# Performance work log

Measured on AMD Instinct MI355X. Metric: run time of the kernel, lower is better.

## Reference

```python
import jax, jax.numpy as jnp
import numpy as np
from jax import lax

B, HIST, FC, N, F = 64, 24, 24, 1000, 8
EMB, HID, NEMB, OUT = 32, 64, 1000, 1
IN = EMB + OUT  # GRU input dim


def setup_inputs() -> dict:
    key = jax.random.key(0)
    ks = jax.random.split(key, 11)
    X = jax.random.normal(ks[0], (B, HIST + FC, N, F), jnp.float32)
    idx = jax.random.randint(ks[1], (B, HIST + FC, N), 0, NEMB)
    X = X.at[..., -1].set(idx.astype(jnp.float32))  # last channel = spatial ids
    hn = jax.random.normal(ks[2], (B * N, HID), jnp.float32)
    xn = jax.random.normal(ks[3], (B, N, OUT), jnp.float32)
    s = 0.1
    emb_table = jax.random.normal(ks[4], (NEMB, EMB), jnp.float32) * s
    W_ih = jax.random.normal(ks[5], (3 * HID, IN), jnp.float32) * s
    W_hh = jax.random.normal(ks[6], (3 * HID, HID), jnp.float32) * s
    b_ih = jax.random.normal(ks[7], (3 * HID,), jnp.float32) * s
    b_hh = jax.random.normal(ks[8], (3 * HID,), jnp.float32) * s
    W_out = jax.random.normal(ks[9], (OUT, HID), jnp.float32) * s
    b_out = jax.random.normal(ks[10], (OUT,), jnp.float32) * s
    return {"X": X, "hn": hn, "xn": xn, "emb_table": emb_table,
            "W_ih": W_ih, "W_hh": W_hh, "b_ih": b_ih, "b_hh": b_hh,
            "W_out": W_out, "b_out": b_out}


def reference(X, hn, xn, emb_table, W_ih, W_hh, b_ih, b_hh, W_out, b_out):
    # indices for the forecast steps: [FC, B, N]
    idx_seq = X[:, :FC, :, -1].astype(jnp.int32).transpose(1, 0, 2)

    def step(carry, idx_t):
        h, x_prev = carry                      # h: [B*N, HID], x_prev: [B, N, 1]
        emb = emb_table[idx_t]                 # [B, N, EMB] gather
        x = jnp.concatenate([x_prev, emb], axis=-1).reshape(B * N, IN)
        gi = x @ W_ih.T + b_ih                 # [B*N, 3*HID]
        gh = h @ W_hh.T + b_hh
        i_r, i_z, i_n = jnp.split(gi, 3, axis=-1)
        h_r, h_z, h_n = jnp.split(gh, 3, axis=-1)
        r = jax.nn.sigmoid(i_r + h_r)
        z = jax.nn.sigmoid(i_z + h_z)
        n = jnp.tanh(i_n + r * h_n)
        h_new = (1.0 - z) * n + z * h
        out = h_new.reshape(B, N, HID) @ W_out.T + b_out  # [B, N, 1]
        return (h_new, out), out

    _, preds = lax.scan(step, (hn, xn), idx_seq)  # preds: [FC, B, N, 1]
    return preds.transpose(1, 0, 2, 3)            # [B, FC, N, 1]
```

## Files before the change

kernel.cpp:

```cpp
#include <hip/hip_runtime.h>
#include <math.h>

#define BB   64
#define FC   24
#define NN   1000
#define HID  64
#define EMBD 32
#define TT   48
#define FF   8
#define NEMB 1000
#define G3   192
#define INSZ 33

#define CPB  32
#define TPB  256
#define MT   2
#define AST  72
#define XST  32

typedef __attribute__((ext_vector_type(8))) short bf16x8;
typedef __attribute__((ext_vector_type(4))) float f32x4;

static __device__ __forceinline__ unsigned short f2bf(float f) {
    unsigned u = __builtin_bit_cast(unsigned, f);
    u += 0x7FFFu + ((u >> 16) & 1u);
    return (unsigned short)(u >> 16);
}
static __device__ __forceinline__ unsigned cvt_pk_bf16(float a, float b) {
    unsigned r;
    asm("v_cvt_pk_bf16_f32 %0, %1, %2" : "=v"(r) : "v"(a), "v"(b));
    return r;
}
static __device__ __forceinline__ float fast_sigmoid(float v) {
    float e = __builtin_amdgcn_exp2f(-1.4426950408889634f * v);
    return __builtin_amdgcn_rcpf(1.0f + e);
}
static __device__ __forceinline__ float fast_tanh(float v) {
    float vv = fminf(fmaxf(v, -15.0f), 15.0f);
    float e = __builtin_amdgcn_exp2f(2.8853900817779268f * vv);
    return 1.0f - 2.0f * __builtin_amdgcn_rcpf(e + 1.0f);
}

static __device__ __forceinline__ void lds_barrier() {
    __builtin_amdgcn_sched_barrier(0);
    asm volatile("s_waitcnt lgkmcnt(0)" ::: "memory");
    __builtin_amdgcn_s_barrier();
    __builtin_amdgcn_sched_barrier(0);
}

__global__ __launch_bounds__(TPB) __attribute__((amdgpu_waves_per_eu(3)))
void gru_decoder(
    const float* __restrict__ X,
    const float* __restrict__ hn0,
    const float* __restrict__ xn,
    const float* __restrict__ emb,
    const float* __restrict__ Wih,
    const float* __restrict__ Whh,
    const float* __restrict__ bih,
    const float* __restrict__ bhh,
    const float* __restrict__ Wout,
    const float* __restrict__ bout,
    float* __restrict__ out)
{
    __shared__ __align__(16) unsigned short Abuf[CPB * AST];
    __shared__ __align__(16) unsigned short Xt[2][CPB * XST];
    __shared__ int   idxbuf[FC * CPB];
    __shared__ float xbuf[CPB];

    const int tid  = threadIdx.x;
    const int lane = tid & 63;
    const int g    = tid >> 6;
    const int quad = lane >> 4;
    const int l15  = lane & 15;
    const int jcol = g * 16 + l15;
    const int rowb = quad * 4;
    const int cell0 = blockIdx.x * CPB;

    for (int e = tid; e < FC * CPB; e += TPB) {
        int t = e >> 5, m = e & 31;
        int cell = cell0 + m;
        int b = cell / NN, n = cell - b * NN;
        idxbuf[t * CPB + m] = (int)X[(((size_t)b * TT + t) * NN + n) * FF + 7];
    }
    if (tid < CPB) xbuf[tid] = xn[cell0 + tid];

    bf16x8 Bf[3][2];
    #pragma unroll
    for (int gate = 0; gate < 3; ++gate) {
        #pragma unroll
        for (int ks = 0; ks < 2; ++ks) {
            const float* src = Whh + (size_t)(gate * HID + jcol) * HID + ks * 32 + quad * 8;
            float4 lo = *(const float4*)src;
            float4 hi = *(const float4*)(src + 4);
            bf16x8 f;
            f[0] = (short)f2bf(lo.x); f[1] = (short)f2bf(lo.y);
            f[2] = (short)f2bf(lo.z); f[3] = (short)f2bf(lo.w);
            f[4] = (short)f2bf(hi.x); f[5] = (short)f2bf(hi.y);
            f[6] = (short)f2bf(hi.z); f[7] = (short)f2bf(hi.w);
            Bf[gate][ks] = f;
        }
    }
    bf16x8 BX[3];
    #pragma unroll
    for (int gate = 0; gate < 3; ++gate) {
        const float* src = Wih + (size_t)(gate * HID + jcol) * INSZ + 1 + quad * 8;
        bf16x8 f;
        #pragma unroll
        for (int e = 0; e < 8; ++e) f[e] = (short)f2bf(src[e]);
        BX[gate] = f;
    }

    const float w0r = Wih[(size_t)jcol * INSZ];
    const float w0z = Wih[(size_t)(HID + jcol) * INSZ];
    const float w0n = Wih[(size_t)(2 * HID + jcol) * INSZ];
    const float br  = bih[jcol] + bhh[jcol];
    const float bz  = bih[HID + jcol] + bhh[HID + jcol];
    const float bni = bih[2 * HID + jcol];
    const float bhn = bhh[2 * HID + jcol];
    const f32x4 cr  = {br,  br,  br,  br };
    const f32x4 cz  = {bz,  bz,  bz,  bz };
    const f32x4 cni = {bni, bni, bni, bni};
    const f32x4 cng = {bhn, bhn, bhn, bhn};
    const float bout0 = bout[0];

    const int cd_m   = g * 8 + (lane & 7);
    const int kslice = lane >> 3;
    float wout_r[8];
    #pragma unroll
    for (int e2 = 0; e2 < 8; ++e2) wout_r[e2] = Wout[kslice * 8 + e2];
    const int cd_cell = cell0 + cd_m;
    const int cd_b = cd_cell / NN, cd_n = cd_cell - cd_b * NN;
    const size_t obase = (size_t)cd_b * FC * NN + cd_n;

    float hold[MT][4];
    #pragma unroll
    for (int mt = 0; mt < MT; ++mt) {
        #pragma unroll
        for (int rr = 0; rr < 4; ++rr) {
            int m = mt * 16 + rowb + rr;
            float h = hn0[((size_t)cell0 + m) * HID + jcol];
            hold[mt][rr] = h;
            Abuf[m * AST + jcol] = f2bf(h);
        }
    }
    __syncthreads();

    const int r8 = tid >> 3, k4 = (tid & 7) * 4;
    {
        int idx = idxbuf[r8];
        float4 e4 = *(const float4*)(emb + (size_t)idx * EMBD + k4);
        unsigned p0 = cvt_pk_bf16(e4.x, e4.y);
        unsigned p1 = cvt_pk_bf16(e4.z, e4.w);
        *(uint2*)&Xt[0][r8 * XST + k4] = make_uint2(p0, p1);
    }
    __syncthreads();

    for (int t = 0; t < FC; ++t) {
        const int tn = (t + 1 < FC) ? t + 1 : FC - 1;
        const int nidx = idxbuf[tn * CPB + r8];
        const float4 e4 = *(const float4*)(emb + (size_t)nidx * EMBD + k4);

        const unsigned short* Xc = Xt[t & 1];

        f32x4 accr[MT], accz[MT], accni[MT], accng[MT];
        #pragma unroll
        for (int mt = 0; mt < MT; ++mt) {
            const bf16x8 a0 = *(const bf16x8*)&Abuf[(mt * 16 + l15) * AST + quad * 8];
            const bf16x8 a1 = *(const bf16x8*)&Abuf[(mt * 16 + l15) * AST + 32 + quad * 8];
            const bf16x8 x0 = *(const bf16x8*)&Xc[(mt * 16 + l15) * XST + quad * 8];
            accr[mt]  = __builtin_amdgcn_mfma_f32_16x16x32_bf16(x0, BX[0], cr, 0, 0, 0);
            accr[mt]  = __builtin_amdgcn_mfma_f32_16x16x32_bf16(a0, Bf[0][0], accr[mt], 0, 0, 0);
            accr[mt]  = __builtin_amdgcn_mfma_f32_16x16x32_bf16(a1, Bf[0][1], accr[mt], 0, 0, 0);
            accz[mt]  = __builtin_amdgcn_mfma_f32_16x16x32_bf16(x0, BX[1], cz, 0, 0, 0);
            accz[mt]  = __builtin_amdgcn_mfma_f32_16x16x32_bf16(a0, Bf[1][0], accz[mt], 0, 0, 0);
            accz[mt]  = __builtin_amdgcn_mfma_f32_16x16x32_bf16(a1, Bf[1][1], accz[mt], 0, 0, 0);
            accni[mt] = __builtin_amdgcn_mfma_f32_16x16x32_bf16(x0, BX[2], cni, 0, 0, 0);
            accng[mt] = __builtin_amdgcn_mfma_f32_16x16x32_bf16(a0, Bf[2][0], cng, 0, 0, 0);
            accng[mt] = __builtin_amdgcn_mfma_f32_16x16x32_bf16(a1, Bf[2][1], accng[mt], 0, 0, 0);
        }

        if (t > 0) {
            bf16x8 hv = *(const bf16x8*)&Abuf[cd_m * AST + kslice * 8];
            const unsigned* hv32 = (const unsigned*)&hv;
            float o = 0.f;
            #pragma unroll
            for (int q = 0; q < 4; ++q) {
                unsigned v = hv32[q];
                o = fmaf(wout_r[2 * q],     __builtin_bit_cast(float, v << 16),         o);
                o = fmaf(wout_r[2 * q + 1], __builtin_bit_cast(float, v & 0xFFFF0000u), o);
            }
            o += __shfl_xor(o, 8);
            o += __shfl_xor(o, 16);
            o += __shfl_xor(o, 32);
            if (lane < 8) {
                float oo = o + bout0;
                out[obase + (size_t)(t - 1) * NN] = oo;
                xbuf[cd_m] = oo;
            }
        }
        lds_barrier();

        #pragma unroll
        for (int mt = 0; mt < MT; ++mt) {
            #pragma unroll
            for (int rp = 0; rp < 2; ++rp) {
                float h2[2];
                #pragma unroll
                for (int k = 0; k < 2; ++k) {
                    const int rr = rp * 2 + k;
                    const int m  = mt * 16 + rowb + rr;
                    float xp = xbuf[m];
                    float r  = fast_sigmoid(fmaf(w0r, xp, accr[mt][rr]));
                    float z  = fast_sigmoid(fmaf(w0z, xp, accz[mt][rr]));
                    float nv = fast_tanh(fmaf(r, accng[mt][rr],
                                              fmaf(w0n, xp, accni[mt][rr])));
                    float hnew = nv + z * (hold[mt][rr] - nv);
                    hold[mt][rr] = hnew;
                    h2[k] = hnew;
                }
                unsigned pk = cvt_pk_bf16(h2[0], h2[1]);
                const int m0 = mt * 16 + rowb + rp * 2;
                Abuf[m0 * AST + jcol]       = (unsigned short)pk;
                Abuf[(m0 + 1) * AST + jcol] = (unsigned short)(pk >> 16);
            }
        }

        {
            unsigned p0 = cvt_pk_bf16(e4.x, e4.y);
            unsigned p1 = cvt_pk_bf16(e4.z, e4.w);
            *(uint2*)&Xt[(t + 1) & 1][r8 * XST + k4] = make_uint2(p0, p1);
        }
        lds_barrier();
    }

    {
        bf16x8 hv = *(const bf16x8*)&Abuf[cd_m * AST + kslice * 8];
        const unsigned* hv32 = (const unsigned*)&hv;
        float o = 0.f;
        #pragma unroll
        for (int q = 0; q < 4; ++q) {
            unsigned v = hv32[q];
            o = fmaf(wout_r[2 * q],     __builtin_bit_cast(float, v << 16),         o);
            o = fmaf(wout_r[2 * q + 1], __builtin_bit_cast(float, v & 0xFFFF0000u), o);
        }
        o += __shfl_xor(o, 8);
        o += __shfl_xor(o, 16);
        o += __shfl_xor(o, 32);
        if (lane < 8) out[obase + (size_t)(FC - 1) * NN] = o + bout0;
    }
}

extern "C" void kernel_launch(void* const* d_in, const int* in_sizes, int n_in,
                              void* d_out, int out_size, void* d_ws, size_t ws_size,
                              hipStream_t stream) {
    (void)in_sizes; (void)n_in; (void)out_size; (void)d_ws; (void)ws_size;
    const float* X    = (const float*)d_in[0];
    const float* hn   = (const float*)d_in[1];
    const float* xn   = (const float*)d_in[2];
    const float* emb  = (const float*)d_in[3];
    const float* Wih  = (const float*)d_in[4];
    const float* Whh  = (const float*)d_in[5];
    const float* bih  = (const float*)d_in[6];
    const float* bhh  = (const float*)d_in[7];
    const float* Wout = (const float*)d_in[8];
    const float* bout = (const float*)d_in[9];
    float* out = (float*)d_out;

    const int blocks = (BB * NN) / CPB;
    gru_decoder<<<blocks, TPB, 0, stream>>>(X, hn, xn, emb, Wih, Whh,
                                            bih, bhh, Wout, bout, out);
}
```

Baseline: 265.1 us.

## Software-pipeline GRU row halves across barriers and fold log2e into weights

```diff
diff --git a/kernel.cpp b/kernel.cpp
--- a/kernel.cpp
+++ b/kernel.cpp
@@ -8,15 +8,15 @@
 #define EMBD 32
 #define TT   48
 #define FF   8
-#define NEMB 1000
-#define G3   192
 #define INSZ 33
 
 #define CPB  32
 #define TPB  256
-#define MT   2
 #define AST  72
-#define XST  32
+#define XST  40
+
+#define NL2E (-1.4426950408889634f)
+#define TL2E ( 2.8853900817779268f)
 
 typedef __attribute__((ext_vector_type(8))) short bf16x8;
 typedef __attribute__((ext_vector_type(4))) float f32x4;
@@ -31,14 +31,13 @@
     asm("v_cvt_pk_bf16_f32 %0, %1, %2" : "=v"(r) : "v"(a), "v"(b));
     return r;
 }
-static __device__ __forceinline__ float fast_sigmoid(float v) {
-    float e = __builtin_amdgcn_exp2f(-1.4426950408889634f * v);
-    return __builtin_amdgcn_rcpf(1.0f + e);
-}
-static __device__ __forceinline__ float fast_tanh(float v) {
-    float vv = fminf(fmaxf(v, -15.0f), 15.0f);
-    float e = __builtin_amdgcn_exp2f(2.8853900817779268f * vv);
-    return 1.0f - 2.0f * __builtin_amdgcn_rcpf(e + 1.0f);
+static __device__ __forceinline__ bf16x8 mk_bf8(float4 lo, float4 hi, float s) {
+    union { unsigned u[4]; bf16x8 v; } r;
+    r.u[0] = cvt_pk_bf16(lo.x * s, lo.y * s);
+    r.u[1] = cvt_pk_bf16(lo.z * s, lo.w * s);
+    r.u[2] = cvt_pk_bf16(hi.x * s, hi.y * s);
+    r.u[3] = cvt_pk_bf16(hi.z * s, hi.w * s);
+    return r.v;
 }
 
 static __device__ __forceinline__ void lds_barrier() {
@@ -87,61 +86,55 @@
     bf16x8 Bf[3][2];
     #pragma unroll
     for (int gate = 0; gate < 3; ++gate) {
+        const float s = (gate < 2) ? NL2E : TL2E;
         #pragma unroll
         for (int ks = 0; ks < 2; ++ks) {
             const float* src = Whh + (size_t)(gate * HID + jcol) * HID + ks * 32 + quad * 8;
-            float4 lo = *(const float4*)src;
-            float4 hi = *(const float4*)(src + 4);
-            bf16x8 f;
-            f[0] = (short)f2bf(lo.x); f[1] = (short)f2bf(lo.y);
-            f[2] = (short)f2bf(lo.z); f[3] = (short)f2bf(lo.w);
-            f[4] = (short)f2bf(hi.x); f[5] = (short)f2bf(hi.y);
-            f[6] = (short)f2bf(hi.z); f[7] = (short)f2bf(hi.w);
-            Bf[gate][ks] = f;
+            Bf[gate][ks] = mk_bf8(*(const float4*)src, *(const float4*)(src + 4), s);
         }
     }
     bf16x8 BX[3];
     #pragma unroll
     for (int gate = 0; gate < 3; ++gate) {
+        const float s = (gate < 2) ? NL2E : TL2E;
         const float* src = Wih + (size_t)(gate * HID + jcol) * INSZ + 1 + quad * 8;
-        bf16x8 f;
+        union { unsigned u[4]; bf16x8 v; } f;
         #pragma unroll
-        for (int e = 0; e < 8; ++e) f[e] = (short)f2bf(src[e]);
-        BX[gate] = f;
-    }
-
-    const float w0r = Wih[(size_t)jcol * INSZ];
-    const float w0z = Wih[(size_t)(HID + jcol) * INSZ];
-    const float w0n = Wih[(size_t)(2 * HID + jcol) * INSZ];
-    const float br  = bih[jcol] + bhh[jcol];
-    const float bz  = bih[HID + jcol] + bhh[HID + jcol];
-    const float bni = bih[2 * HID + jcol];
-    const float bhn = bhh[2 * HID + jcol];
-    const f32x4 cr  = {br,  br,  br,  br };
-    const f32x4 cz  = {bz,  bz,  bz,  bz };
-    const f32x4 cni = {bni, bni, bni, bni};
-    const f32x4 cng = {bhn, bhn, bhn, bhn};
+        for (int p = 0; p < 4; ++p)
+            f.u[p] = cvt_pk_bf16(src[2 * p] * s, src[2 * p + 1] * s);
+        BX[gate] = f.v;
+    }
+
+    const float w0r2 = NL2E * Wih[(size_t)jcol * INSZ];
+    const float w0z2 = NL2E * Wih[(size_t)(HID + jcol) * INSZ];
+    const float w0n2 = TL2E * Wih[(size_t)(2 * HID + jcol) * INSZ];
+    const float br2  = NL2E * (bih[jcol] + bhh[jcol]);
+    const float bz2  = NL2E * (bih[HID + jcol] + bhh[HID + jcol]);
+    const float bni2 = TL2E * bih[2 * HID + jcol];
+    const float bhn2 = TL2E * bhh[2 * HID + jcol];
     const float bout0 = bout[0];
 
-    const int cd_m   = g * 8 + (lane & 7);
-    const int kslice = lane >> 3;
-    float wout_r[8];
-    #pragma unroll
-    for (int e2 = 0; e2 < 8; ++e2) wout_r[e2] = Wout[kslice * 8 + e2];
-    const int cd_cell = cell0 + cd_m;
-    const int cd_b = cd_cell / NN, cd_n = cd_cell - cd_b * NN;
-    const size_t obase = (size_t)cd_b * FC * NN + cd_n;
-
-    float hold[MT][4];
-    #pragma unroll
-    for (int mt = 0; mt < MT; ++mt) {
-        #pragma unroll
-        for (int rr = 0; rr < 4; ++rr) {
-            int m = mt * 16 + rowb + rr;
-            float h = hn0[((size_t)cell0 + m) * HID + jcol];
-            hold[mt][rr] = h;
-            Abuf[m * AST + jcol] = f2bf(h);
-        }
+    float wout4[4];
+    #pragma unroll
+    for (int e2 = 0; e2 < 4; ++e2) wout4[e2] = Wout[l15 * 4 + e2];
+    const int od_c = g * 4 + quad;
+    size_t ob[2];
+    #pragma unroll
+    for (int gx = 0; gx < 2; ++gx) {
+        int cell = cell0 + gx * 16 + od_c;
+        int b = cell / NN, n = cell - b * NN;
+        ob[gx] = (size_t)b * FC * NN + n;
+    }
+
+    float hold0[4], hold1[4];
+    #pragma unroll
+    for (int rr = 0; rr < 4; ++rr) {
+        int m0 = rowb + rr, m1 = 16 + rowb + rr;
+        float h0 = hn0[((size_t)cell0 + m0) * HID + jcol];
+        float h1 = hn0[((size_t)cell0 + m1) * HID + jcol];
+        hold0[rr] = h0; hold1[rr] = h1;
+        Abuf[m0 * AST + jcol] = f2bf(h0);
+        Abuf[m1 * AST + jcol] = f2bf(h1);
     }
     __syncthreads();
 
@@ -149,105 +142,104 @@
     {
         int idx = idxbuf[r8];
         float4 e4 = *(const float4*)(emb + (size_t)idx * EMBD + k4);
-        unsigned p0 = cvt_pk_bf16(e4.x, e4.y);
-        unsigned p1 = cvt_pk_bf16(e4.z, e4.w);
-        *(uint2*)&Xt[0][r8 * XST + k4] = make_uint2(p0, p1);
+        *(uint2*)&Xt[0][r8 * XST + k4] =
+            make_uint2(cvt_pk_bf16(e4.x, e4.y), cvt_pk_bf16(e4.z, e4.w));
     }
     __syncthreads();
 
+    auto PHASE_A = [&](int X16, const unsigned short* Xc,
+                       f32x4& ar, f32x4& az, f32x4& ani, f32x4& ang) {
+        const bf16x8 a0 = *(const bf16x8*)&Abuf[(X16 + l15) * AST + quad * 8];
+        const bf16x8 a1 = *(const bf16x8*)&Abuf[(X16 + l15) * AST + 32 + quad * 8];
+        const bf16x8 x0 = *(const bf16x8*)&Xc[(X16 + l15) * XST + quad * 8];
+        const f32x4 z4 = {0.f, 0.f, 0.f, 0.f};
+        ar  = __builtin_amdgcn_mfma_f32_16x16x32_bf16(x0, BX[0], z4, 0, 0, 0);
+        ar  = __builtin_amdgcn_mfma_f32_16x16x32_bf16(a0, Bf[0][0], ar, 0, 0, 0);
+        ar  = __builtin_amdgcn_mfma_f32_16x16x32_bf16(a1, Bf[0][1], ar, 0, 0, 0);
+        az  = __builtin_amdgcn_mfma_f32_16x16x32_bf16(x0, BX[1], z4, 0, 0, 0);
+        az  = __builtin_amdgcn_mfma_f32_16x16x32_bf16(a0, Bf[1][0], az, 0, 0, 0);
+        az  = __builtin_amdgcn_mfma_f32_16x16x32_bf16(a1, Bf[1][1], az, 0, 0, 0);
+        ani = __builtin_amdgcn_mfma_f32_16x16x32_bf16(x0, BX[2], z4, 0, 0, 0);
+        ang = __builtin_amdgcn_mfma_f32_16x16x32_bf16(a0, Bf[2][0], z4, 0, 0, 0);
+        ang = __builtin_amdgcn_mfma_f32_16x16x32_bf16(a1, Bf[2][1], ang, 0, 0, 0);
+    };
+
+    auto PHASE_B = [&](int X16, f32x4& ar, f32x4& az, f32x4& ani, f32x4& ang,
+                       float* hold) {
+        #pragma unroll
+        for (int rp = 0; rp < 2; ++rp) {
+            float h2[2];
+            #pragma unroll
+            for (int k = 0; k < 2; ++k) {
+                const int rr = rp * 2 + k;
+                const int m  = X16 + rowb + rr;
+                const float xp = xbuf[m];
+                float sr = fmaf(w0r2, xp, ar[rr] + br2);
+                float r  = __builtin_amdgcn_rcpf(1.0f + __builtin_amdgcn_exp2f(sr));
+                float sz = fmaf(w0z2, xp, az[rr] + bz2);
+                float z  = __builtin_amdgcn_rcpf(1.0f + __builtin_amdgcn_exp2f(sz));
+                float v  = fmaf(r, ang[rr] + bhn2, fmaf(w0n2, xp, ani[rr] + bni2));
+                float e  = __builtin_amdgcn_exp2f(v);
+                float nv = fmaf(-2.0f, __builtin_amdgcn_rcpf(e + 1.0f), 1.0f);
+                float hnew = fmaf(z, hold[rr] - nv, nv);
+                hold[rr] = hnew;
+                h2[k] = hnew;
+            }
+            unsigned pk = cvt_pk_bf16(h2[0], h2[1]);
+            const int m0 = X16 + rowb + rp * 2;
+            Abuf[m0 * AST + jcol]       = (unsigned short)pk;
+            Abuf[(m0 + 1) * AST + jcol] = (unsigned short)(pk >> 16);
+        }
+    };
+
+    auto OUTDOT = [&](int gx, int tw, bool wr) {
+        const int X16 = gx << 4;
+        const uint2 hv = *(const uint2*)&Abuf[(X16 + od_c) * AST + l15 * 4];
+        float o;
+        o = wout4[0] * __builtin_bit_cast(float, hv.x << 16);
+        o = fmaf(wout4[1], __builtin_bit_cast(float, hv.x & 0xFFFF0000u), o);
+        o = fmaf(wout4[2], __builtin_bit_cast(float, hv.y << 16), o);
+        o = fmaf(wout4[3], __builtin_bit_cast(float, hv.y & 0xFFFF0000u), o);
+        o += __shfl_xor(o, 1);
+        o += __shfl_xor(o, 2);
+        o += __shfl_xor(o, 4);
+        o += __shfl_xor(o, 8);
+        if (l15 == 0) {
+            float oo = o + bout0;
+            out[ob[gx] + (size_t)tw * NN] = oo;
+            if (wr) xbuf[X16 + od_c] = oo;
+        }
+    };
+
+    f32x4 ar0, az0, ani0, ang0;
+    f32x4 ar1, az1, ani1, ang1;
+
+    #pragma unroll 2
     for (int t = 0; t < FC; ++t) {
         const int tn = (t + 1 < FC) ? t + 1 : FC - 1;
         const int nidx = idxbuf[tn * CPB + r8];
         const float4 e4 = *(const float4*)(emb + (size_t)nidx * EMBD + k4);
-
         const unsigned short* Xc = Xt[t & 1];
 
-        f32x4 accr[MT], accz[MT], accni[MT], accng[MT];
-        #pragma unroll
-        for (int mt = 0; mt < MT; ++mt) {
-            const bf16x8 a0 = *(const bf16x8*)&Abuf[(mt * 16 + l15) * AST + quad * 8];
-            const bf16x8 a1 = *(const bf16x8*)&Abuf[(mt * 16 + l15) * AST + 32 + quad * 8];
-            const bf16x8 x0 = *(const bf16x8*)&Xc[(mt * 16 + l15) * XST + quad * 8];
-            accr[mt]  = __builtin_amdgcn_mfma_f32_16x16x32_bf16(x0, BX[0], cr, 0, 0, 0);
-            accr[mt]  = __builtin_amdgcn_mfma_f32_16x16x32_bf16(a0, Bf[0][0], accr[mt], 0, 0, 0);
-            accr[mt]  = __builtin_amdgcn_mfma_f32_16x16x32_bf16(a1, Bf[0][1], accr[mt], 0, 0, 0);
-            accz[mt]  = __builtin_amdgcn_mfma_f32_16x16x32_bf16(x0, BX[1], cz, 0, 0, 0);
-            accz[mt]  = __builtin_amdgcn_mfma_f32_16x16x32_bf16(a0, Bf[1][0], accz[mt], 0, 0, 0);
-            accz[mt]  = __builtin_amdgcn_mfma_f32_16x16x32_bf16(a1, Bf[1][1], accz[mt], 0, 0, 0);
-            accni[mt] = __builtin_amdgcn_mfma_f32_16x16x32_bf16(x0, BX[2], cni, 0, 0, 0);
-            accng[mt] = __builtin_amdgcn_mfma_f32_16x16x32_bf16(a0, Bf[2][0], cng, 0, 0, 0);
-            accng[mt] = __builtin_amdgcn_mfma_f32_16x16x32_bf16(a1, Bf[2][1], accng[mt], 0, 0, 0);
-        }
-
+        PHASE_A(0, Xc, ar0, az0, ani0, ang0);
         if (t > 0) {
-            bf16x8 hv = *(const bf16x8*)&Abuf[cd_m * AST + kslice * 8];
-            const unsigned* hv32 = (const unsigned*)&hv;
-            float o = 0.f;
-            #pragma unroll
-            for (int q = 0; q < 4; ++q) {
-                unsigned v = hv32[q];
-                o = fmaf(wout_r[2 * q],     __builtin_bit_cast(float, v << 16),         o);
-                o = fmaf(wout_r[2 * q + 1], __builtin_bit_cast(float, v & 0xFFFF0000u), o);
-            }
-            o += __shfl_xor(o, 8);
-            o += __shfl_xor(o, 16);
-            o += __shfl_xor(o, 32);
-            if (lane < 8) {
-                float oo = o + bout0;
-                out[obase + (size_t)(t - 1) * NN] = oo;
-                xbuf[cd_m] = oo;
-            }
+            PHASE_B(16, ar1, az1, ani1, ang1, hold1);
+            OUTDOT(0, t - 1, true);
         }
         lds_barrier();
 
-        #pragma unroll
-        for (int mt = 0; mt < MT; ++mt) {
-            #pragma unroll
-            for (int rp = 0; rp < 2; ++rp) {
-                float h2[2];
-                #pragma unroll
-                for (int k = 0; k < 2; ++k) {
-                    const int rr = rp * 2 + k;
-                    const int m  = mt * 16 + rowb + rr;
-                    float xp = xbuf[m];
-                    float r  = fast_sigmoid(fmaf(w0r, xp, accr[mt][rr]));
-                    float z  = fast_sigmoid(fmaf(w0z, xp, accz[mt][rr]));
-                    float nv = fast_tanh(fmaf(r, accng[mt][rr],
-                                              fmaf(w0n, xp, accni[mt][rr])));
-                    float hnew = nv + z * (hold[mt][rr] - nv);
-                    hold[mt][rr] = hnew;
-                    h2[k] = hnew;
-                }
-                unsigned pk = cvt_pk_bf16(h2[0], h2[1]);
-                const int m0 = mt * 16 + rowb + rp * 2;
-                Abuf[m0 * AST + jcol]       = (unsigned short)pk;
-                Abuf[(m0 + 1) * AST + jcol] = (unsigned short)(pk >> 16);
-            }
-        }
-
-        {
-            unsigned p0 = cvt_pk_bf16(e4.x, e4.y);
-            unsigned p1 = cvt_pk_bf16(e4.z, e4.w);
-            *(uint2*)&Xt[(t + 1) & 1][r8 * XST + k4] = make_uint2(p0, p1);
-        }
+        PHASE_A(16, Xc, ar1, az1, ani1, ang1);
+        PHASE_B(0, ar0, az0, ani0, ang0, hold0);
+        if (t > 0) OUTDOT(1, t - 1, true);
+        *(uint2*)&Xt[(t + 1) & 1][r8 * XST + k4] =
+            make_uint2(cvt_pk_bf16(e4.x, e4.y), cvt_pk_bf16(e4.z, e4.w));
         lds_barrier();
     }
 
-    {
-        bf16x8 hv = *(const bf16x8*)&Abuf[cd_m * AST + kslice * 8];
-        const unsigned* hv32 = (const unsigned*)&hv;
-        float o = 0.f;
-        #pragma unroll
-        for (int q = 0; q < 4; ++q) {
-            unsigned v = hv32[q];
-            o = fmaf(wout_r[2 * q],     __builtin_bit_cast(float, v << 16),         o);
-            o = fmaf(wout_r[2 * q + 1], __builtin_bit_cast(float, v & 0xFFFF0000u), o);
-        }
-        o += __shfl_xor(o, 8);
-        o += __shfl_xor(o, 16);
-        o += __shfl_xor(o, 32);
-        if (lane < 8) out[obase + (size_t)(FC - 1) * NN] = o + bout0;
-    }
+    PHASE_B(16, ar1, az1, ani1, ang1, hold1);
+    OUTDOT(0, FC - 1, false);
+    lds_barrier();
+    OUTDOT(1, FC - 1, false);
 }
 
 extern "C" void kernel_launch(void* const* d_in, const int* in_sizes, int n_in,
```

New measurement: 274.6 us. 1.04x slower.
